# Kernel optimization log

Measured on AMD Instinct MI355X. Metric: run time of the kernel, lower is better.

The kernel has to match this reference:

```python
import jax, jax.numpy as jnp
import numpy as np

B, S, FDIM = 8, 512, 512
SUB = 4
DIM = FDIM // SUB            # 128 (reformer model dim)
HEADS, LOCAL_HEADS = 8, 2
LSH_HEADS = HEADS - LOCAL_HEADS
DH = 64                      # dim_head
INNER = HEADS * DH           # 512
BUCKET = 64
N_HASHES = 4
MEM = 128                    # num_mem_kv
DEPTH = 2                    # cfg.selfatn.num_layers
T = S * SUB + MEM            # 2176 internal seq (tokens + mem kv)
NB = T // BUCKET             # 34 buckets (even)
WINDOW = BUCKET * 2          # local attention window = 128
SELF_VAL = -5e4              # TOKEN_SELF_ATTN_VALUE
NEG = -1e9


def _ln(x, g, b, eps=1e-5):
    m = jnp.mean(x, -1, keepdims=True)
    v = jnp.mean((x - m) ** 2, -1, keepdims=True)
    return (x - m) * jax.lax.rsqrt(v + eps) * g + b


def _pos_encoding(s, d):
    pos = jnp.arange(s, dtype=jnp.float32)[:, None]
    i = jnp.arange(d, dtype=jnp.float32)
    div = 10000.0 ** (2.0 * i / d)
    pe = jnp.zeros((s, d), jnp.float32)
    pe = pe.at[:, 0::2].set(jnp.sin(pos / div[0::2]))
    pe = pe.at[:, 1::2].set(jnp.cos(pos / div[1::2]))
    return pe


def _l2norm(x, eps=1e-12):
    n = jnp.linalg.norm(x, axis=-1, keepdims=True)
    return x / jnp.maximum(n, eps)


def _lsh_attn(qk, v, rot):
    # qk, v: [Bh, T, DH]; rot: [DH, N_HASHES, NB//2] random rotations
    Bh, t, d = qk.shape
    rv = jnp.einsum('btf,fhi->bhti', qk, rot)
    rv = jnp.concatenate([rv, -rv], axis=-1)               # [Bh, nh, t, NB]
    buckets = jnp.argmax(rv, axis=-1)
    buckets = buckets + (jnp.arange(N_HASHES) * NB)[None, :, None]
    buckets = buckets.reshape(Bh, N_HASHES * t)
    ticker = jnp.arange(N_HASHES * t) % t
    key = buckets * t + ticker                             # sort by (bucket, pos)
    perm = jnp.argsort(key, axis=-1)                       # stable
    undo = jnp.argsort(perm, axis=-1)
    st = perm % t                                          # source positions
    sqk = jnp.take_along_axis(qk, st[..., None], axis=1)
    sv = jnp.take_along_axis(v, st[..., None], axis=1)
    C = N_HASHES * NB
    bq_t = st.reshape(Bh, C, BUCKET)
    bq = sqk.reshape(Bh, C, BUCKET, d)
    bv = sv.reshape(Bh, C, BUCKET, d)
    bk = _l2norm(bq)                                       # shared-QK: normalized keys
    look = lambda x: jnp.concatenate([x, jnp.roll(x, 1, axis=1)], axis=2)
    bk, bv, bkv_t = look(bk), look(bv), look(bq_t)
    dots = jnp.einsum('bcie,bcje->bcij', bq, bk) * (d ** -0.5)
    dots = jnp.where(bq_t[..., None] < bkv_t[:, :, None, :], NEG, dots)      # causal
    dots = jnp.where(bq_t[..., None] == bkv_t[:, :, None, :], SELF_VAL, dots)  # self
    lse = jax.nn.logsumexp(dots, axis=-1, keepdims=True)
    bo = jnp.einsum('bcij,bcje->bcie', jnp.exp(dots - lse), bv)
    so = bo.reshape(Bh, N_HASHES * t, d)
    slog = lse.reshape(Bh, N_HASHES * t)
    o = jnp.take_along_axis(so, undo[..., None], axis=1).reshape(Bh, N_HASHES, t, d)
    logits = jnp.take_along_axis(slog, undo, axis=1).reshape(Bh, N_HASHES, t, 1)
    w = jnp.exp(logits - jax.nn.logsumexp(logits, axis=1, keepdims=True))
    return (o * w).sum(axis=1)


def _local_attn(q, v):
    # shared-QK causal local attention, look_backward=1; q, v: [Bh, T, DH]
    Bh, t, d = q.shape
    W = t // WINDOW
    k = _l2norm(q)
    bq = q.reshape(Bh, W, WINDOW, d)
    bk = k.reshape(Bh, W, WINDOW, d)
    bv = v.reshape(Bh, W, WINDOW, d)
    tt = jnp.arange(t).reshape(W, WINDOW)
    prev = lambda x: jnp.concatenate([jnp.zeros_like(x[:, :1]), x[:, :-1]], axis=1)
    bk2 = jnp.concatenate([prev(bk), bk], axis=2)          # [Bh, W, 2W, d]
    bv2 = jnp.concatenate([prev(bv), bv], axis=2)
    tprev = jnp.concatenate([jnp.full((1, WINDOW), -1), tt[:-1]], axis=0)
    bkv_t = jnp.concatenate([tprev, tt], axis=1)           # [W, 2*WINDOW]
    dots = jnp.einsum('bwie,bwje->bwij', bq, bk2) * (d ** -0.5)
    dots = jnp.where(tt[:, :, None] == bkv_t[:, None, :], SELF_VAL, dots)
    dots = jnp.where(tt[:, :, None] < bkv_t[:, None, :], NEG, dots)
    dots = jnp.where((bkv_t == -1)[:, None, :], NEG, dots)
    attn = jax.nn.softmax(dots, axis=-1)
    return jnp.einsum('bwij,bwje->bwie', attn, bv2).reshape(Bh, t, d)


def _attn_layer(x, w_qk, w_v, mem_kv, w_out, b_out, rot):
    b, t0, _ = x.shape
    mem = jnp.broadcast_to(mem_kv, (b, MEM, DIM))
    xm = jnp.concatenate([x, mem], axis=1)                 # [b, T, DIM]
    qk = (xm @ w_qk).reshape(b, T, HEADS, DH).transpose(0, 2, 1, 3)
    v = (xm @ w_v).reshape(b, T, HEADS, DH).transpose(0, 2, 1, 3)
    merge = lambda a: a.reshape(-1, T, DH)
    out_loc = _local_attn(merge(qk[:, :LOCAL_HEADS]), merge(v[:, :LOCAL_HEADS]))
    out_lsh = _lsh_attn(merge(qk[:, LOCAL_HEADS:]), merge(v[:, LOCAL_HEADS:]), rot)
    out = jnp.concatenate([out_loc.reshape(b, LOCAL_HEADS, T, DH),
                           out_lsh.reshape(b, LSH_HEADS, T, DH)], axis=1)
    out = out.transpose(0, 2, 1, 3).reshape(b, T, INNER)
    return out[:, :t0] @ w_out + b_out


def setup_inputs() -> dict:
    key = jax.random.key(0)
    ks = jax.random.split(key, 20)
    std = 0.01  # init_network truncated-normal std
    p = lambda k, sh: std * jax.random.truncated_normal(k, -2.0, 2.0, sh, jnp.float32)
    return {
        'features': jax.random.normal(ks[0], (B, S, FDIM), jnp.float32),
        'w_qk': p(ks[1], (DEPTH, DIM, INNER)),
        'w_v': p(ks[2], (DEPTH, DIM, INNER)),
        'mem_kv': p(ks[3], (DEPTH, MEM, DIM)),
        'w_out': p(ks[4], (DEPTH, INNER, DIM)),
        'b_out': p(ks[5], (DEPTH, DIM)),
        'ln1_g': jnp.ones((DEPTH, DIM), jnp.float32),
        'ln1_b': jnp.zeros((DEPTH, DIM), jnp.float32),
        'ff_w1': p(ks[6], (DEPTH, DIM, 4 * DIM)),
        'ff_b1': p(ks[7], (DEPTH, 4 * DIM)),
        'ff_w2': p(ks[8], (DEPTH, 4 * DIM, DIM)),
        'ff_b2': p(ks[9], (DEPTH, DIM)),
        'ln2_g': jnp.ones((DEPTH, DIM), jnp.float32),
        'ln2_b': jnp.zeros((DEPTH, DIM), jnp.float32),
        'lnf_g': jnp.ones((DIM,), jnp.float32),
        'lnf_b': jnp.zeros((DIM,), jnp.float32),
        'rotations': jax.random.normal(ks[10], (DEPTH, DH, N_HASHES, NB // 2), jnp.float32),
    }


def reference(features, w_qk, w_v, mem_kv, w_out, b_out, ln1_g, ln1_b,
              ff_w1, ff_b1, ff_w2, ff_b2, ln2_g, ln2_b, lnf_g, lnf_b, rotations):
    b, s, fd = features.shape
    x = features + _pos_encoding(s, fd)                    # PositionalEncoding
    x = x.reshape(b, s * SUB, fd // SUB)                   # subspace split
    # reversible Reformer blocks: y1 = x1 + attn(ln(x2)); y2 = x2 + ff(ln(y1))
    x1, x2 = x, x
    for i in range(DEPTH):
        a_in = _ln(x2, ln1_g[i], ln1_b[i])
        y1 = x1 + _attn_layer(a_in, w_qk[i], w_v[i], mem_kv[i], w_out[i], b_out[i], rotations[i])
        g_in = _ln(y1, ln2_g[i], ln2_b[i])
        h = jax.nn.gelu(g_in @ ff_w1[i] + ff_b1[i], approximate=False)
        y2 = x2 + (h @ ff_w2[i] + ff_b2[i])
        x1, x2 = y1, y2
    x = 0.5 * (x1 + x2)                                    # mean of the two streams
    x = _ln(x, lnf_g, lnf_b)                               # final norm
    x = x.reshape(b, s, fd)                                # merge subspaces back
    return x.mean(axis=1)                                  # AvgPool
```

## Files before the change

### kernel.cpp

```cpp
#include <hip/hip_runtime.h>
#include <math.h>

#define NB_ 34
#define NEGV  (-1e9f)
#define SELFV (-5e4f)

typedef __attribute__((ext_vector_type(8))) short short8;
typedef __attribute__((ext_vector_type(4))) float floatx4;

__device__ __forceinline__ unsigned short f2bf(float f) {
  unsigned int u = __float_as_uint(f);
  u += 0x7fffu + ((u >> 16) & 1u);
  return (unsigned short)(u >> 16);
}
__device__ __forceinline__ float bflo(unsigned int u) { return __uint_as_float(u << 16); }
__device__ __forceinline__ float bfhi(unsigned int u) { return __uint_as_float(u & 0xffff0000u); }

__device__ __forceinline__ void load_row64(const float* __restrict__ p, float* q) {
#pragma unroll
  for (int d4 = 0; d4 < 16; ++d4) {
    float4 f = ((const float4*)p)[d4];
    q[d4*4+0]=f.x; q[d4*4+1]=f.y; q[d4*4+2]=f.z; q[d4*4+3]=f.w;
  }
}


__global__ void pos_kernel(const float* __restrict__ feat, float* __restrict__ x1,
                           float* __restrict__ x2) {
  int idx = blockIdx.x*256 + threadIdx.x;
  int d = idx & 127, t = (idx >> 7) & 2047, b = idx >> 18;
  int s = t >> 2, c = ((t & 3) << 7) | d;
  float div = powf(10000.0f, (float)c * (1.0f/256.0f));
  float arg = (float)s / div;
  float pe = (c & 1) ? cosf(arg) : sinf(arg);
  float val = feat[((size_t)b*512 + s)*512 + c] + pe;
  x1[idx] = val; x2[idx] = val;
}

__global__ __launch_bounds__(256) void ln_kernel(
    const float* __restrict__ in, const float* __restrict__ in2,
    const float* __restrict__ g, const float* __restrict__ bta,
    void* __restrict__ out, int rows, int ou, int oa, int obf) {
  int wid = threadIdx.x >> 6, lane = threadIdx.x & 63;
  int row = blockIdx.x*4 + wid;
  if (row >= rows) return;
  float2 x = ((const float2*)(in + (size_t)row*128))[lane];
  if (in2) {
    float2 y = ((const float2*)(in2 + (size_t)row*128))[lane];
    x.x = 0.5f*(x.x + y.x); x.y = 0.5f*(x.y + y.y);
  }
  float s = x.x + x.y;
#pragma unroll
  for (int m = 1; m < 64; m <<= 1) s += __shfl_xor(s, m, 64);
  float mean = s * (1.0f/128.0f);
  float dx = x.x - mean, dy = x.y - mean;
  float v = dx*dx + dy*dy;
#pragma unroll
  for (int m = 1; m < 64; m <<= 1) v += __shfl_xor(v, m, 64);
  float inv = 1.0f / sqrtf(v*(1.0f/128.0f) + 1e-5f);
  int orow = (ou == oa) ? row : (row/ou)*oa + (row%ou);
  float2 gg = ((const float2*)g)[lane];
  float2 bb = ((const float2*)bta)[lane];
  float ox = dx*inv*gg.x + bb.x, oy = dy*inv*gg.y + bb.y;
  if (obf) {
    ((unsigned int*)out)[(size_t)orow*64 + lane] =
        (unsigned int)f2bf(ox) | ((unsigned int)f2bf(oy) << 16);
  } else {
    float2 o; o.x = ox; o.y = oy;
    ((float2*)((float*)out + (size_t)orow*128))[lane] = o;
  }
}

__global__ void memfill_kernel(const float* __restrict__ mem,
                               unsigned short* __restrict__ xmb) {
  int idx = blockIdx.x*256 + threadIdx.x;
  int d = idx & 127, r = (idx >> 7) & 127, b = idx >> 14;
  xmb[((size_t)b*2176 + 2048 + r)*128 + d] = f2bf(mem[(r << 7) | d]);
}

__global__ void wconv_kernel(const float* __restrict__ w, unsigned short* __restrict__ wt,
                             int K, int N) {
  int idx = blockIdx.x*256 + threadIdx.x;
  int k = idx % K, n = idx / K;
  wt[idx] = f2bf(w[(size_t)k*N + n]);
}

__global__ __launch_bounds__(256) void gemm_bf16(
    const unsigned short* __restrict__ A, const unsigned short* __restrict__ Wt,
    const float* __restrict__ bias, const float* __restrict__ resid,
    float* __restrict__ C, unsigned short* __restrict__ Cb,
    int M, int N, int K, int au, int aa, int act) {
  __shared__ __align__(16) unsigned short As[64*40];
  __shared__ __align__(16) unsigned short Bs[64*40];
  int tid = threadIdx.x;
  int wid = tid >> 6, l15 = tid & 15, quad = (tid & 63) >> 4;
  int mb = blockIdx.y, nb = blockIdx.x;
  int r = tid >> 2, cc = (tid & 3)*8;
  int rg = mb*64 + r;
  int rp = (au == aa) ? rg : (rg/au)*aa + (rg%au);
  const unsigned short* arow = A + (size_t)rp*K + cc;
  const unsigned short* brow = Wt + (size_t)(nb*64 + r)*K + cc;
  floatx4 acc[4];
#pragma unroll
  for (int mt = 0; mt < 4; ++mt) acc[mt] = (floatx4){0.f,0.f,0.f,0.f};
  for (int k0 = 0; k0 < K; k0 += 32) {
    *(short8*)&As[r*40 + cc] = *(const short8*)(arow + k0);
    *(short8*)&Bs[r*40 + cc] = *(const short8*)(brow + k0);
    __syncthreads();
    short8 bfr = *(const short8*)&Bs[(wid*16 + l15)*40 + quad*8];
#pragma unroll
    for (int mt = 0; mt < 4; ++mt) {
      short8 afr = *(const short8*)&As[(mt*16 + l15)*40 + quad*8];
      acc[mt] = __builtin_amdgcn_mfma_f32_16x16x32_bf16(afr, bfr, acc[mt], 0, 0, 0);
    }
    __syncthreads();
  }
  int n = nb*64 + wid*16 + l15;
  float bi = bias ? bias[n] : 0.f;
#pragma unroll
  for (int mt = 0; mt < 4; ++mt) {
#pragma unroll
    for (int rr = 0; rr < 4; ++rr) {
      int m = mb*64 + mt*16 + quad*4 + rr;
      float val = acc[mt][rr] + bi;
      if (act) val = 0.5f*val*(1.0f + erff(val*0.70710678118654752f));
      if (resid) val += resid[(size_t)m*N + n];
      if (Cb) Cb[(size_t)m*N + n] = f2bf(val);
      else    C[(size_t)m*N + n] = val;
    }
  }
}

__global__ __launch_bounds__(128) void local_attn_mfma(
    const float* __restrict__ qk, const unsigned short* __restrict__ vbb,
    unsigned short* __restrict__ opart, float* __restrict__ lpart) {
  __shared__ __align__(16) unsigned short qq[128*72];
  __shared__ __align__(16) unsigned short kk[128*72];
  __shared__ __align__(16) unsigned short vt[64*136];
  __shared__ __align__(16) unsigned short ptile[2][16*136];
  __shared__ float invn[128];

  int blk = blockIdx.x;
  int part = blk & 1;
  int bw = blk >> 1;
  int bh = bw / 17, w = bw % 17;
  int b = bh >> 1, coloff = (bh & 1)*64;
  int tid = threadIdx.x;
  int t_qbase = w*128;

  unsigned short* obase = opart + (size_t)(part*16 + bh)*2176*64;
  float* lbase = lpart + (size_t)(part*16 + bh)*2176;

  if (part == 0 && w == 0) {
    uint4 z = {0,0,0,0};
    uint4* orow = (uint4*)(obase + (size_t)tid*64);
#pragma unroll
    for (int j = 0; j < 8; ++j) orow[j] = z;
    lbase[tid] = -1e9f;
    return;
  }

  {
    int t = t_qbase + tid;
    const float* qr = qk + ((size_t)(b*2176 + t)*512 + coloff);
    float ss = 0.f;
#pragma unroll
    for (int k8 = 0; k8 < 8; ++k8) {
      float4 a = ((const float4*)qr)[2*k8];
      float4 c = ((const float4*)qr)[2*k8+1];
      ss += a.x*a.x + a.y*a.y + a.z*a.z + a.w*a.w
          + c.x*c.x + c.y*c.y + c.z*c.z + c.w*c.w;
      short8 s8;
      s8[0]=(short)f2bf(a.x); s8[1]=(short)f2bf(a.y);
      s8[2]=(short)f2bf(a.z); s8[3]=(short)f2bf(a.w);
      s8[4]=(short)f2bf(c.x); s8[5]=(short)f2bf(c.y);
      s8[6]=(short)f2bf(c.z); s8[7]=(short)f2bf(c.w);
      *(short8*)&qq[tid*72 + k8*8] = s8;
    }
    if (part) invn[tid] = 1.0f / fmaxf(sqrtf(ss), 1e-12f);
  }
  if (part == 0) {
    int t = t_qbase - 128 + tid;
    const float* qr = qk + ((size_t)(b*2176 + t)*512 + coloff);
    float ss = 0.f;
#pragma unroll
    for (int k8 = 0; k8 < 8; ++k8) {
      float4 a = ((const float4*)qr)[2*k8];
      float4 c = ((const float4*)qr)[2*k8+1];
      ss += a.x*a.x + a.y*a.y + a.z*a.z + a.w*a.w
          + c.x*c.x + c.y*c.y + c.z*c.z + c.w*c.w;
      short8 s8;
      s8[0]=(short)f2bf(a.x); s8[1]=(short)f2bf(a.y);
      s8[2]=(short)f2bf(a.z); s8[3]=(short)f2bf(a.w);
      s8[4]=(short)f2bf(c.x); s8[5]=(short)f2bf(c.y);
      s8[6]=(short)f2bf(c.z); s8[7]=(short)f2bf(c.w);
      *(short8*)&kk[tid*72 + k8*8] = s8;
    }
    invn[tid] = 1.0f / fmaxf(sqrtf(ss), 1e-12f);
  }
  if (tid < 64) {
    int tkb = part ? t_qbase : (t_qbase - 128);
    const unsigned short* vrA = vbb + ((size_t)(b*2176 + tkb + 2*tid)*512 + coloff);
    const unsigned short* vrB = vrA + 512;
    unsigned int* vt32 = (unsigned int*)vt;
#pragma unroll
    for (int k = 0; k < 8; ++k) {
      uint4 ua = ((const uint4*)vrA)[k];
      uint4 uc = ((const uint4*)vrB)[k];
      const unsigned short* pa = (const unsigned short*)&ua;
      const unsigned short* pc = (const unsigned short*)&uc;
#pragma unroll
      for (int j = 0; j < 8; ++j) {
        int d = 8*k + j;
        vt32[d*68 + tid] = (unsigned int)pa[j] | ((unsigned int)pc[j] << 16);
      }
    }
  }
  __syncthreads();

  int wid = tid >> 6, l15 = tid & 15, quad = (tid & 63) >> 4;
  const unsigned short* keyrows = part ? qq : kk;
  int tkbase = part ? t_qbase : (t_qbase - 128);
  float sm8[8];
#pragma unroll
  for (int nt = 0; nt < 8; ++nt) sm8[nt] = invn[nt*16 + l15] * 0.125f;
  int qrow0 = wid*64;
  unsigned short* pt = &ptile[wid][0];

#pragma unroll
  for (int mt = 0; mt < 4; ++mt) {
    floatx4 acc[8];
#pragma unroll
    for (int nt = 0; nt < 8; ++nt) acc[nt] = (floatx4){0.f,0.f,0.f,0.f};
#pragma unroll
    for (int ks = 0; ks < 2; ++ks) {
      short8 afr = *(const short8*)&qq[(qrow0 + mt*16 + l15)*72 + ks*32 + quad*8];
#pragma unroll
      for (int nt = 0; nt < 8; ++nt) {
        short8 bfr = *(const short8*)&keyrows[(nt*16 + l15)*72 + ks*32 + quad*8];
        acc[nt] = __builtin_amdgcn_mfma_f32_16x16x32_bf16(afr, bfr, acc[nt], 0, 0, 0);
      }
    }
    float invl[4];
#pragma unroll
    for (int r = 0; r < 4; ++r) {
      int row = qrow0 + mt*16 + quad*4 + r;
      int t_q = t_qbase + row;
      float sv[8]; float mx = -INFINITY;
#pragma unroll
      for (int nt = 0; nt < 8; ++nt) {
        float sc = acc[nt][r] * sm8[nt];
        int t_k = tkbase + nt*16 + l15;
        sc = (t_k > t_q) ? NEGV : (t_k == t_q ? SELFV : sc);
        sv[nt] = sc; mx = fmaxf(mx, sc);
      }
#pragma unroll
      for (int m2 = 1; m2 < 16; m2 <<= 1) mx = fmaxf(mx, __shfl_xor(mx, m2, 64));
      float l = 0.f;
#pragma unroll
      for (int nt = 0; nt < 8; ++nt) { float pe = expf(sv[nt] - mx); sv[nt] = pe; l += pe; }
#pragma unroll
      for (int m2 = 1; m2 < 16; m2 <<= 1) l += __shfl_xor(l, m2, 64);
      invl[r] = 1.0f / l;
#pragma unroll
      for (int nt = 0; nt < 8; ++nt)
        pt[(quad*4 + r)*136 + nt*16 + l15] = f2bf(sv[nt]);
      if (l15 == 0) lbase[t_q] = mx + logf(l);
    }
#pragma unroll
    for (int nt = 0; nt < 4; ++nt) {
      floatx4 po = (floatx4){0.f,0.f,0.f,0.f};
#pragma unroll
      for (int ks = 0; ks < 4; ++ks) {
        short8 afr = *(const short8*)&pt[l15*136 + ks*32 + quad*8];
        short8 bfr = *(const short8*)&vt[(nt*16 + l15)*136 + ks*32 + quad*8];
        po = __builtin_amdgcn_mfma_f32_16x16x32_bf16(afr, bfr, po, 0, 0, 0);
      }
      int d = nt*16 + l15;
#pragma unroll
      for (int r = 0; r < 4; ++r) {
        int t_q = t_qbase + qrow0 + mt*16 + quad*4 + r;
        obase[(size_t)t_q*64 + d] = f2bf(po[r] * invl[r]);
      }
    }
  }
}

__global__ void local_comb(const unsigned short* __restrict__ opart,
                           const float* __restrict__ lpart,
                           unsigned short* __restrict__ aob) {
  int idx = blockIdx.x*256 + threadIdx.x;
  if (idx >= 16*2176*8) return;
  int f8 = idx & 7;
  int p  = (idx >> 3) % 2176;
  int bh = idx / (8*2176);
  float lg0 = lpart[(size_t)bh*2176 + p];
  float lg1 = lpart[(size_t)(16 + bh)*2176 + p];
  float m = fmaxf(lg0, lg1);
  float e0 = expf(lg0 - m), e1 = expf(lg1 - m);
  float inv = 1.0f / (e0 + e1);
  float w0 = e0*inv, w1 = e1*inv;
  uint4 u0 = ((const uint4*)(opart + ((size_t)bh*2176 + p)*64))[f8];
  uint4 u1 = ((const uint4*)(opart + ((size_t)(16 + bh)*2176 + p)*64))[f8];
  uint4 o;
  o.x = (unsigned int)f2bf(w0*bflo(u0.x) + w1*bflo(u1.x)) |
        ((unsigned int)f2bf(w0*bfhi(u0.x) + w1*bfhi(u1.x)) << 16);
  o.y = (unsigned int)f2bf(w0*bflo(u0.y) + w1*bflo(u1.y)) |
        ((unsigned int)f2bf(w0*bfhi(u0.y) + w1*bfhi(u1.y)) << 16);
  o.z = (unsigned int)f2bf(w0*bflo(u0.z) + w1*bflo(u1.z)) |
        ((unsigned int)f2bf(w0*bfhi(u0.z) + w1*bfhi(u1.z)) << 16);
  o.w = (unsigned int)f2bf(w0*bflo(u0.w) + w1*bflo(u1.w)) |
        ((unsigned int)f2bf(w0*bfhi(u0.w) + w1*bfhi(u1.w)) << 16);
  int b = bh >> 1;
  ((uint4*)(aob + ((size_t)(b*2176 + p)*512 + (bh & 1)*64 + f8*8)))[0] = o;
}

__global__ __launch_bounds__(256) void hash_kernel(
    const float* __restrict__ qk, const float* __restrict__ rot, int* __restrict__ bucket) {
  __shared__ float rl[64*68];
  for (int l = threadIdx.x; l < 4352; l += 256) rl[l] = rot[l];
  __syncthreads();
  int idx = blockIdx.x*256 + threadIdx.x;
  int p = idx % 2176, bh = idx / 2176;
  int b = bh / 6, hh = bh % 6;
  float q[64];
  load_row64(qk + ((size_t)(b*2176 + p)*512 + (2+hh)*64), q);
  for (int h = 0; h < 4; ++h) {
    float rv[17];
#pragma unroll
    for (int k = 0; k < 17; ++k) rv[k] = 0.f;
    for (int d = 0; d < 64; ++d) {
      float qd = q[d];
      const float* rp = &rl[d*68 + h*17];
#pragma unroll
      for (int k = 0; k < 17; ++k) rv[k] = fmaf(qd, rp[k], rv[k]);
    }
    float best = rv[0]; int bi = 0;
#pragma unroll
    for (int k = 1; k < 34; ++k) {
      float val = (k < 17) ? rv[k] : -rv[k-17];
      if (val > best) { best = val; bi = k; }
    }
    bucket[(size_t)(bh*4 + h)*2176 + p] = bi;
  }
}

__global__ __launch_bounds__(256) void sort_kernel(const int* __restrict__ bucket,
                                                   int* __restrict__ st) {
  __shared__ int sb[2176];
  __shared__ int cnt[NB_*256];
  __shared__ int csum[256];
  int tid = threadIdx.x;
  int bhh = blockIdx.x;
  const int* bin = bucket + (size_t)bhh*2176;
  for (int p = tid; p < 2176; p += 256) sb[p] = bin[p];
#pragma unroll
  for (int j = 0; j < NB_; ++j) cnt[j*256 + tid] = 0;
  __syncthreads();
  int s0 = tid*9;
  int e = s0 + 9; if (e > 2176) e = 2176;
  for (int p = s0; p < e; ++p) cnt[sb[p]*256 + tid] += 1;
  __syncthreads();
  {
    int sum = 0;
    int base0 = tid*NB_;
#pragma unroll
    for (int j = 0; j < NB_; ++j) {
      int v = cnt[base0 + j];
      cnt[base0 + j] = sum;
      sum += v;
    }
    csum[tid] = sum;
  }
  __syncthreads();
  for (int off = 1; off < 256; off <<= 1) {
    int v = (tid >= off) ? csum[tid - off] : 0;
    __syncthreads();
    csum[tid] += v;
    __syncthreads();
  }
  {
    int base = tid ? csum[tid-1] : 0;
    int base0 = tid*NB_;
#pragma unroll
    for (int j = 0; j < NB_; ++j) cnt[base0 + j] += base;
  }
  __syncthreads();
  int bh = bhh >> 2, h = bhh & 3;
  int* outp = st + (size_t)bh*8704 + h*2176;
  for (int p = s0; p < e; ++p) {
    int bk = sb[p];
    int r = cnt[bk*256 + tid]++;
    outp[r] = p;
  }
}

__global__ __launch_bounds__(128) void lsh_attn_mfma(
    const float* __restrict__ qk, const unsigned short* __restrict__ vbb,
    const int* __restrict__ st, unsigned short* __restrict__ o_all,
    float* __restrict__ logits) {
  __shared__ __align__(16) unsigned short qq[192*72];
  __shared__ __align__(16) unsigned short vt[64*200];
  __shared__ __align__(16) unsigned short ptile[2][16*136];
  __shared__ int   tkl[192];
  __shared__ float invn[192];

  int blk = blockIdx.x;
  int bh = blk / 68, pair = blk % 68;
  int c0 = pair*2;
  int b = bh / 6, coloff = (2 + bh % 6)*64;
  int tid = threadIdx.x;

#pragma unroll
  for (int rr = 0; rr < 2; ++rr) {
    if (rr == 1 && tid >= 64) break;
    int r = (rr == 0) ? tid : 128 + tid;
    int cr = c0 - 1 + (r >> 6); if (cr < 0) cr += 136;
    int p = st[(size_t)bh*8704 + cr*64 + (r & 63)];
    tkl[r] = p;
    const float* qr = qk + ((size_t)(b*2176 + p)*512 + coloff);
    float ss = 0.f;
#pragma unroll
    for (int k8 = 0; k8 < 8; ++k8) {
      float4 a = ((const float4*)qr)[2*k8];
      float4 c = ((const float4*)qr)[2*k8+1];
      ss += a.x*a.x + a.y*a.y + a.z*a.z + a.w*a.w
          + c.x*c.x + c.y*c.y + c.z*c.z + c.w*c.w;
      short8 s8;
      s8[0]=(short)f2bf(a.x); s8[1]=(short)f2bf(a.y);
      s8[2]=(short)f2bf(a.z); s8[3]=(short)f2bf(a.w);
      s8[4]=(short)f2bf(c.x); s8[5]=(short)f2bf(c.y);
      s8[6]=(short)f2bf(c.z); s8[7]=(short)f2bf(c.w);
      *(short8*)&qq[r*72 + k8*8] = s8;
    }
    invn[r] = 1.0f / fmaxf(sqrtf(ss), 1e-12f);
  }
  if (tid < 96) {
    int r0 = 2*tid, r1 = r0 + 1;
    int cr0 = c0 - 1 + (r0 >> 6); if (cr0 < 0) cr0 += 136;
    int cr1 = c0 - 1 + (r1 >> 6); if (cr1 < 0) cr1 += 136;
    int p0 = st[(size_t)bh*8704 + cr0*64 + (r0 & 63)];
    int p1 = st[(size_t)bh*8704 + cr1*64 + (r1 & 63)];
    const unsigned short* a = vbb + ((size_t)(b*2176 + p0)*512 + coloff);
    const unsigned short* c = vbb + ((size_t)(b*2176 + p1)*512 + coloff);
    unsigned int* vt32 = (unsigned int*)vt;
#pragma unroll
    for (int k = 0; k < 8; ++k) {
      uint4 ua = ((const uint4*)a)[k];
      uint4 uc = ((const uint4*)c)[k];
      const unsigned short* pa = (const unsigned short*)&ua;
      const unsigned short* pc = (const unsigned short*)&uc;
#pragma unroll
      for (int j = 0; j < 8; ++j) {
        int d = 8*k + j;
        vt32[d*100 + tid] = (unsigned int)pa[j] | ((unsigned int)pc[j] << 16);
      }
    }
  }
  __syncthreads();

  int wid = tid >> 6, l15 = tid & 15, quad = (tid & 63) >> 4;
  int kbase = wid*64, qbase = 64 + wid*64;
  int c = c0 + wid;
  int h = c / NB_;
  float sm8[8]; int tk8[8];
#pragma unroll
  for (int nt = 0; nt < 8; ++nt) {
    int kr = kbase + nt*16 + l15;
    sm8[nt] = invn[kr] * 0.125f;
    tk8[nt] = tkl[kr];
  }
  float* logrow = logits + (size_t)(bh*4 + h)*2176;
  unsigned short* obase = o_all + (size_t)(bh*4 + h)*2176*64;
  unsigned short* pt = &ptile[wid][0];

#pragma unroll
  for (int mt = 0; mt < 4; ++mt) {
    floatx4 acc[8];
#pragma unroll
    for (int nt = 0; nt < 8; ++nt) acc[nt] = (floatx4){0.f,0.f,0.f,0.f};
#pragma unroll
    for (int ks = 0; ks < 2; ++ks) {
      short8 afr = *(const short8*)&qq[(qbase + mt*16 + l15)*72 + ks*32 + quad*8];
#pragma unroll
      for (int nt = 0; nt < 8; ++nt) {
        short8 bfr = *(const short8*)&qq[(kbase + nt*16 + l15)*72 + ks*32 + quad*8];
        acc[nt] = __builtin_amdgcn_mfma_f32_16x16x32_bf16(afr, bfr, acc[nt], 0, 0, 0);
      }
    }
    float invl[4];
#pragma unroll
    for (int r = 0; r < 4; ++r) {
      int t_q = tkl[qbase + mt*16 + quad*4 + r];
      float sv8[8]; float mx = -INFINITY;
#pragma unroll
      for (int nt = 0; nt < 8; ++nt) {
        float sc = acc[nt][r] * sm8[nt];
        int t_k = tk8[nt];
        sc = (t_k > t_q) ? NEGV : (t_k == t_q ? SELFV : sc);
        sv8[nt] = sc; mx = fmaxf(mx, sc);
      }
#pragma unroll
      for (int m2 = 1; m2 < 16; m2 <<= 1) mx = fmaxf(mx, __shfl_xor(mx, m2, 64));
      float l = 0.f;
#pragma unroll
      for (int nt = 0; nt < 8; ++nt) { float pe = expf(sv8[nt] - mx); sv8[nt] = pe; l += pe; }
#pragma unroll
      for (int m2 = 1; m2 < 16; m2 <<= 1) l += __shfl_xor(l, m2, 64);
      invl[r] = 1.0f / l;
#pragma unroll
      for (int nt = 0; nt < 8; ++nt)
        pt[(quad*4 + r)*136 + nt*16 + l15] = f2bf(sv8[nt]);
      if (l15 == 0) logrow[t_q] = mx + logf(l);
    }
#pragma unroll
    for (int nt = 0; nt < 4; ++nt) {
      floatx4 po = (floatx4){0.f,0.f,0.f,0.f};
#pragma unroll
      for (int ks = 0; ks < 4; ++ks) {
        short8 afr = *(const short8*)&pt[l15*136 + ks*32 + quad*8];
        short8 bfr = *(const short8*)&vt[(nt*16 + l15)*200 + kbase + ks*32 + quad*8];
        po = __builtin_amdgcn_mfma_f32_16x16x32_bf16(afr, bfr, po, 0, 0, 0);
      }
      int d = nt*16 + l15;
#pragma unroll
      for (int r = 0; r < 4; ++r) {
        int p_q = tkl[qbase + mt*16 + quad*4 + r];
        obase[(size_t)p_q*64 + d] = f2bf(po[r] * invl[r]);
      }
    }
  }
}

__global__ void comb_kernel(const unsigned short* __restrict__ o_all,
                            const float* __restrict__ logits,
                            unsigned short* __restrict__ aob) {
  int idx = blockIdx.x*256 + threadIdx.x;
  int f8 = idx & 7;
  int p  = (idx >> 3) % 2176;
  int bh = idx / (8*2176);
  float lg0 = logits[(size_t)(bh*4+0)*2176 + p];
  float lg1 = logits[(size_t)(bh*4+1)*2176 + p];
  float lg2 = logits[(size_t)(bh*4+2)*2176 + p];
  float lg3 = logits[(size_t)(bh*4+3)*2176 + p];
  float m = fmaxf(fmaxf(lg0, lg1), fmaxf(lg2, lg3));
  float e0 = expf(lg0-m), e1 = expf(lg1-m), e2 = expf(lg2-m), e3 = expf(lg3-m);
  float inv = 1.0f / (e0+e1+e2+e3);
  float wh[4] = {e0*inv, e1*inv, e2*inv, e3*inv};
  float o[8];
#pragma unroll
  for (int d = 0; d < 8; ++d) o[d] = 0.f;
#pragma unroll
  for (int h = 0; h < 4; ++h) {
    float wg = wh[h];
    uint4 u = ((const uint4*)(o_all + ((size_t)(bh*4+h)*2176 + p)*64))[f8];
    o[0] = fmaf(wg, bflo(u.x), o[0]); o[1] = fmaf(wg, bfhi(u.x), o[1]);
    o[2] = fmaf(wg, bflo(u.y), o[2]); o[3] = fmaf(wg, bfhi(u.y), o[3]);
    o[4] = fmaf(wg, bflo(u.z), o[4]); o[5] = fmaf(wg, bfhi(u.z), o[5]);
    o[6] = fmaf(wg, bflo(u.w), o[6]); o[7] = fmaf(wg, bfhi(u.w), o[7]);
  }
  int b = bh / 6, hh = bh % 6;
  uint4 u;
  u.x = (unsigned int)f2bf(o[0]) | ((unsigned int)f2bf(o[1]) << 16);
  u.y = (unsigned int)f2bf(o[2]) | ((unsigned int)f2bf(o[3]) << 16);
  u.z = (unsigned int)f2bf(o[4]) | ((unsigned int)f2bf(o[5]) << 16);
  u.w = (unsigned int)f2bf(o[6]) | ((unsigned int)f2bf(o[7]) << 16);
  ((uint4*)(aob + ((size_t)(b*2176 + p)*512 + (2+hh)*64 + f8*8)))[0] = u;
}

__global__ void pool_kernel(const float* __restrict__ xln, float* __restrict__ out) {
  int idx = blockIdx.x*256 + threadIdx.x;
  int c = idx & 511, b = idx >> 9;
  int sub = c >> 7, d = c & 127;
  const float* p = xln + ((size_t)b*2048 + sub)*128 + d;
  float s = 0.f;
  for (int i = 0; i < 512; ++i) s += p[(size_t)i*512];
  out[idx] = s * (1.0f/512.0f);
}

#define OFF_X1    0ull
#define OFF_X2    2097152ull
#define OFF_XM    4194304ull
#define OFF_XMB   6422528ull
#define OFF_QKB   7536640ull
#define OFF_VB    16449536ull
#define OFF_AOB   25362432ull
#define OFF_OALL  29818880ull
#define OFF_LOG   43188224ull
#define OFF_BKT   43606016ull
#define OFF_ST    44023808ull
#define OFF_WTB   44441600ull
#define WS_FLOATS 44769280ull

extern "C" void kernel_launch(void* const* d_in, const int* in_sizes, int n_in,
                              void* d_out, int out_size, void* d_ws, size_t ws_size,
                              hipStream_t stream) {
  (void)in_sizes; (void)n_in; (void)out_size;
  if (ws_size < WS_FLOATS * 4ull) return;

  const float* feat  = (const float*)d_in[0];
  const float* w_qk  = (const float*)d_in[1];
  const float* w_v   = (const float*)d_in[2];
  const float* memkv = (const float*)d_in[3];
  const float* w_out = (const float*)d_in[4];
  const float* b_out = (const float*)d_in[5];
  const float* ln1g  = (const float*)d_in[6];
  const float* ln1b  = (const float*)d_in[7];
  const float* ffw1  = (const float*)d_in[8];
  const float* ffb1  = (const float*)d_in[9];
  const float* ffw2  = (const float*)d_in[10];
  const float* ffb2  = (const float*)d_in[11];
  const float* ln2g  = (const float*)d_in[12];
  const float* ln2b  = (const float*)d_in[13];
  const float* lnfg  = (const float*)d_in[14];
  const float* lnfb  = (const float*)d_in[15];
  const float* rots  = (const float*)d_in[16];

  float* ws = (float*)d_ws;
  float* x1   = ws + OFF_X1;
  float* x2   = ws + OFF_X2;
  float* xm   = ws + OFF_XM;
  unsigned short* xmb = (unsigned short*)(ws + OFF_XMB);
  float* qkb  = ws + OFF_QKB;
  unsigned short* vbb = (unsigned short*)(ws + OFF_VB);
  unsigned short* aob = (unsigned short*)(ws + OFF_AOB);
  unsigned short* hb  = (unsigned short*)(ws + OFF_AOB);
  unsigned short* oall = (unsigned short*)(ws + OFF_OALL);
  unsigned short* opart = (unsigned short*)(ws + OFF_OALL);
  float* lpart = ws + OFF_OALL + 2228224ull;
  float* logi = ws + OFF_LOG;
  int*   bkt  = (int*)(ws + OFF_BKT);
  int*   st   = (int*)(ws + OFF_ST);
  unsigned short* wtb = (unsigned short*)(ws + OFF_WTB);
  float* outp = (float*)d_out;

  pos_kernel<<<8192, 256, 0, stream>>>(feat, x1, x2);

  for (int i = 0; i < 2; ++i) {
    wconv_kernel<<<256, 256, 0, stream>>>(w_qk + i*65536, wtb + (i*5+0)*65536, 128, 512);
    wconv_kernel<<<256, 256, 0, stream>>>(w_v  + i*65536, wtb + (i*5+1)*65536, 128, 512);
    wconv_kernel<<<256, 256, 0, stream>>>(w_out+ i*65536, wtb + (i*5+2)*65536, 512, 128);
    wconv_kernel<<<256, 256, 0, stream>>>(ffw1 + i*65536, wtb + (i*5+3)*65536, 128, 512);
    wconv_kernel<<<256, 256, 0, stream>>>(ffw2 + i*65536, wtb + (i*5+4)*65536, 512, 128);
  }

  for (int i = 0; i < 2; ++i) {
    const unsigned short* Wqk = wtb + (i*5+0)*65536;
    const unsigned short* Wv  = wtb + (i*5+1)*65536;
    const unsigned short* Wo  = wtb + (i*5+2)*65536;
    const unsigned short* W1  = wtb + (i*5+3)*65536;
    const unsigned short* W2  = wtb + (i*5+4)*65536;

    ln_kernel<<<4096, 256, 0, stream>>>(x2, nullptr, ln1g + i*128, ln1b + i*128,
                                        xmb, 16384, 2048, 2176, 1);
    memfill_kernel<<<512, 256, 0, stream>>>(memkv + i*16384, xmb);

    gemm_bf16<<<dim3(8, 272), 256, 0, stream>>>(xmb, Wqk, nullptr, nullptr, qkb, nullptr,
                                                17408, 512, 128, 1, 1, 0);
    gemm_bf16<<<dim3(8, 272), 256, 0, stream>>>(xmb, Wv, nullptr, nullptr, nullptr, vbb,
                                                17408, 512, 128, 1, 1, 0);

    local_attn_mfma<<<544, 128, 0, stream>>>(qkb, vbb, opart, lpart);
    local_comb<<<1088, 256, 0, stream>>>(opart, lpart, aob);

    hash_kernel<<<408, 256, 0, stream>>>(qkb, rots + i*4352, bkt);
    sort_kernel<<<192, 256, 0, stream>>>(bkt, st);
    lsh_attn_mfma<<<3264, 128, 0, stream>>>(qkb, vbb, st, oall, logi);
    comb_kernel<<<3264, 256, 0, stream>>>(oall, logi, aob);

    gemm_bf16<<<dim3(2, 256), 256, 0, stream>>>(aob, Wo, b_out + i*128, x1, x1, nullptr,
                                                16384, 128, 512, 2048, 2176, 0);
    ln_kernel<<<4096, 256, 0, stream>>>(x1, nullptr, ln2g + i*128, ln2b + i*128,
                                        xmb, 16384, 1, 1, 1);
    gemm_bf16<<<dim3(8, 256), 256, 0, stream>>>(xmb, W1, ffb1 + i*512, nullptr, nullptr, hb,
                                                16384, 512, 128, 1, 1, 1);
    gemm_bf16<<<dim3(2, 256), 256, 0, stream>>>(hb, W2, ffb2 + i*128, x2, x2, nullptr,
                                                16384, 128, 512, 1, 1, 0);
  }

  ln_kernel<<<4096, 256, 0, stream>>>(x1, x2, lnfg, lnfb, xm, 16384, 1, 1, 0);
  pool_kernel<<<16, 256, 0, stream>>>(xm, outp);
}
```

Baseline: 872.0 us.

## Store QK in bf16, fuse QK/V GEMMs, precompute key norms, parallelize pooling

The QK and V projections are merged into one GEMM kernel that writes both outputs in bf16. It relies on the two converted weight blocks sitting next to each other in memory. A separate kernel computes the inverse L2 norm of each QK row once, so the local and LSH attention kernels and the hash kernel no longer reload fp32 rows, recompute norms and convert to bf16. The pooling kernel now uses one wavefront per output with a shuffle reduction instead of a long serial loop per thread. Hashing and norms now read bf16-rounded QK, which can move a few bucket assignments.

```diff
diff --git a/kernel.cpp b/kernel.cpp
--- a/kernel.cpp
+++ b/kernel.cpp
@@ -16,11 +16,14 @@
 __device__ __forceinline__ float bflo(unsigned int u) { return __uint_as_float(u << 16); }
 __device__ __forceinline__ float bfhi(unsigned int u) { return __uint_as_float(u & 0xffff0000u); }
 
-__device__ __forceinline__ void load_row64(const float* __restrict__ p, float* q) {
-#pragma unroll
-  for (int d4 = 0; d4 < 16; ++d4) {
-    float4 f = ((const float4*)p)[d4];
-    q[d4*4+0]=f.x; q[d4*4+1]=f.y; q[d4*4+2]=f.z; q[d4*4+3]=f.w;
+__device__ __forceinline__ void load_row64_bf(const unsigned short* __restrict__ p, float* q) {
+#pragma unroll
+  for (int k = 0; k < 8; ++k) {
+    uint4 u = ((const uint4*)p)[k];
+    q[8*k+0]=bflo(u.x); q[8*k+1]=bfhi(u.x);
+    q[8*k+2]=bflo(u.y); q[8*k+3]=bfhi(u.y);
+    q[8*k+4]=bflo(u.z); q[8*k+5]=bfhi(u.z);
+    q[8*k+6]=bflo(u.w); q[8*k+7]=bfhi(u.w);
   }
 }
 
@@ -131,8 +134,67 @@
   }
 }
 
+__global__ __launch_bounds__(256) void gemm_qv(
+    const unsigned short* __restrict__ A, const unsigned short* __restrict__ Wt,
+    unsigned short* __restrict__ Q, unsigned short* __restrict__ V) {
+  __shared__ __align__(16) unsigned short As[64*40];
+  __shared__ __align__(16) unsigned short Bs[64*40];
+  int tid = threadIdx.x;
+  int wid = tid >> 6, l15 = tid & 15, quad = (tid & 63) >> 4;
+  int mb = blockIdx.y, nb = blockIdx.x;
+  int r = tid >> 2, cc = (tid & 3)*8;
+  const unsigned short* arow = A + (size_t)(mb*64 + r)*128 + cc;
+  const unsigned short* brow = Wt + (size_t)(nb*64 + r)*128 + cc;
+  floatx4 acc[4];
+#pragma unroll
+  for (int mt = 0; mt < 4; ++mt) acc[mt] = (floatx4){0.f,0.f,0.f,0.f};
+#pragma unroll
+  for (int k0 = 0; k0 < 128; k0 += 32) {
+    *(short8*)&As[r*40 + cc] = *(const short8*)(arow + k0);
+    *(short8*)&Bs[r*40 + cc] = *(const short8*)(brow + k0);
+    __syncthreads();
+    short8 bfr = *(const short8*)&Bs[(wid*16 + l15)*40 + quad*8];
+#pragma unroll
+    for (int mt = 0; mt < 4; ++mt) {
+      short8 afr = *(const short8*)&As[(mt*16 + l15)*40 + quad*8];
+      acc[mt] = __builtin_amdgcn_mfma_f32_16x16x32_bf16(afr, bfr, acc[mt], 0, 0, 0);
+    }
+    __syncthreads();
+  }
+  int n = nb*64 + wid*16 + l15;
+#pragma unroll
+  for (int mt = 0; mt < 4; ++mt) {
+#pragma unroll
+    for (int rr = 0; rr < 4; ++rr) {
+      int m = mb*64 + mt*16 + quad*4 + rr;
+      unsigned short bv = f2bf(acc[mt][rr]);
+      if (n < 512) Q[(size_t)m*512 + n] = bv;
+      else         V[(size_t)m*512 + (n - 512)] = bv;
+    }
+  }
+}
+
+__global__ __launch_bounds__(256) void norm_kernel(const unsigned short* __restrict__ qkb,
+                                                   float* __restrict__ nrm) {
+  int idx = blockIdx.x*256 + threadIdx.x;
+  int head = idx & 7, row = idx >> 3;
+  const uint4* src = (const uint4*)(qkb + (size_t)row*512 + head*64);
+  float ss = 0.f;
+#pragma unroll
+  for (int k = 0; k < 8; ++k) {
+    uint4 u = src[k];
+    ss += bflo(u.x)*bflo(u.x) + bfhi(u.x)*bfhi(u.x)
+        + bflo(u.y)*bflo(u.y) + bfhi(u.y)*bfhi(u.y)
+        + bflo(u.z)*bflo(u.z) + bfhi(u.z)*bfhi(u.z)
+        + bflo(u.w)*bflo(u.w) + bfhi(u.w)*bfhi(u.w);
+  }
+  int b = row / 2176, t = row % 2176;
+  nrm[((size_t)b*8 + head)*2176 + t] = 1.0f / fmaxf(sqrtf(ss), 1e-12f);
+}
+
 __global__ __launch_bounds__(128) void local_attn_mfma(
-    const float* __restrict__ qk, const unsigned short* __restrict__ vbb,
+    const unsigned short* __restrict__ qkb, const unsigned short* __restrict__ vbb,
+    const float* __restrict__ nrm,
     unsigned short* __restrict__ opart, float* __restrict__ lpart) {
   __shared__ __align__(16) unsigned short qq[128*72];
   __shared__ __align__(16) unsigned short kk[128*72];
@@ -160,47 +222,22 @@
     return;
   }
 
+  int tkbase = part ? t_qbase : (t_qbase - 128);
+  const float* nrmh = nrm + ((size_t)b*8 + (bh & 1))*2176;
+  invn[tid] = nrmh[tkbase + tid];
+
   {
-    int t = t_qbase + tid;
-    const float* qr = qk + ((size_t)(b*2176 + t)*512 + coloff);
-    float ss = 0.f;
-#pragma unroll
-    for (int k8 = 0; k8 < 8; ++k8) {
-      float4 a = ((const float4*)qr)[2*k8];
-      float4 c = ((const float4*)qr)[2*k8+1];
-      ss += a.x*a.x + a.y*a.y + a.z*a.z + a.w*a.w
-          + c.x*c.x + c.y*c.y + c.z*c.z + c.w*c.w;
-      short8 s8;
-      s8[0]=(short)f2bf(a.x); s8[1]=(short)f2bf(a.y);
-      s8[2]=(short)f2bf(a.z); s8[3]=(short)f2bf(a.w);
-      s8[4]=(short)f2bf(c.x); s8[5]=(short)f2bf(c.y);
-      s8[6]=(short)f2bf(c.z); s8[7]=(short)f2bf(c.w);
-      *(short8*)&qq[tid*72 + k8*8] = s8;
-    }
-    if (part) invn[tid] = 1.0f / fmaxf(sqrtf(ss), 1e-12f);
+    const unsigned short* qr = qkb + ((size_t)(b*2176 + t_qbase + tid)*512 + coloff);
+#pragma unroll
+    for (int k = 0; k < 8; ++k) *(uint4*)&qq[tid*72 + k*8] = ((const uint4*)qr)[k];
   }
   if (part == 0) {
-    int t = t_qbase - 128 + tid;
-    const float* qr = qk + ((size_t)(b*2176 + t)*512 + coloff);
-    float ss = 0.f;
-#pragma unroll
-    for (int k8 = 0; k8 < 8; ++k8) {
-      float4 a = ((const float4*)qr)[2*k8];
-      float4 c = ((const float4*)qr)[2*k8+1];
-      ss += a.x*a.x + a.y*a.y + a.z*a.z + a.w*a.w
-          + c.x*c.x + c.y*c.y + c.z*c.z + c.w*c.w;
-      short8 s8;
-      s8[0]=(short)f2bf(a.x); s8[1]=(short)f2bf(a.y);
-      s8[2]=(short)f2bf(a.z); s8[3]=(short)f2bf(a.w);
-      s8[4]=(short)f2bf(c.x); s8[5]=(short)f2bf(c.y);
-      s8[6]=(short)f2bf(c.z); s8[7]=(short)f2bf(c.w);
-      *(short8*)&kk[tid*72 + k8*8] = s8;
-    }
-    invn[tid] = 1.0f / fmaxf(sqrtf(ss), 1e-12f);
+    const unsigned short* qr = qkb + ((size_t)(b*2176 + t_qbase - 128 + tid)*512 + coloff);
+#pragma unroll
+    for (int k = 0; k < 8; ++k) *(uint4*)&kk[tid*72 + k*8] = ((const uint4*)qr)[k];
   }
   if (tid < 64) {
-    int tkb = part ? t_qbase : (t_qbase - 128);
-    const unsigned short* vrA = vbb + ((size_t)(b*2176 + tkb + 2*tid)*512 + coloff);
+    const unsigned short* vrA = vbb + ((size_t)(b*2176 + tkbase + 2*tid)*512 + coloff);
     const unsigned short* vrB = vrA + 512;
     unsigned int* vt32 = (unsigned int*)vt;
 #pragma unroll
@@ -220,7 +257,6 @@
 
   int wid = tid >> 6, l15 = tid & 15, quad = (tid & 63) >> 4;
   const unsigned short* keyrows = part ? qq : kk;
-  int tkbase = part ? t_qbase : (t_qbase - 128);
   float sm8[8];
 #pragma unroll
   for (int nt = 0; nt < 8; ++nt) sm8[nt] = invn[nt*16 + l15] * 0.125f;
@@ -316,7 +352,8 @@
 }
 
 __global__ __launch_bounds__(256) void hash_kernel(
-    const float* __restrict__ qk, const float* __restrict__ rot, int* __restrict__ bucket) {
+    const unsigned short* __restrict__ qkb, const float* __restrict__ rot,
+    int* __restrict__ bucket) {
   __shared__ float rl[64*68];
   for (int l = threadIdx.x; l < 4352; l += 256) rl[l] = rot[l];
   __syncthreads();
@@ -324,7 +361,7 @@
   int p = idx % 2176, bh = idx / 2176;
   int b = bh / 6, hh = bh % 6;
   float q[64];
-  load_row64(qk + ((size_t)(b*2176 + p)*512 + (2+hh)*64), q);
+  load_row64_bf(qkb + ((size_t)(b*2176 + p)*512 + (2+hh)*64), q);
   for (int h = 0; h < 4; ++h) {
     float rv[17];
 #pragma unroll
@@ -396,9 +433,9 @@
 }
 
 __global__ __launch_bounds__(128) void lsh_attn_mfma(
-    const float* __restrict__ qk, const unsigned short* __restrict__ vbb,
-    const int* __restrict__ st, unsigned short* __restrict__ o_all,
-    float* __restrict__ logits) {
+    const unsigned short* __restrict__ qkb, const unsigned short* __restrict__ vbb,
+    const float* __restrict__ nrm, const int* __restrict__ st,
+    unsigned short* __restrict__ o_all, float* __restrict__ logits) {
   __shared__ __align__(16) unsigned short qq[192*72];
   __shared__ __align__(16) unsigned short vt[64*200];
   __shared__ __align__(16) unsigned short ptile[2][16*136];
@@ -410,6 +447,7 @@
   int c0 = pair*2;
   int b = bh / 6, coloff = (2 + bh % 6)*64;
   int tid = threadIdx.x;
+  const float* nrmh = nrm + ((size_t)b*8 + 2 + bh % 6)*2176;
 
 #pragma unroll
   for (int rr = 0; rr < 2; ++rr) {
@@ -418,22 +456,10 @@
     int cr = c0 - 1 + (r >> 6); if (cr < 0) cr += 136;
     int p = st[(size_t)bh*8704 + cr*64 + (r & 63)];
     tkl[r] = p;
-    const float* qr = qk + ((size_t)(b*2176 + p)*512 + coloff);
-    float ss = 0.f;
-#pragma unroll
-    for (int k8 = 0; k8 < 8; ++k8) {
-      float4 a = ((const float4*)qr)[2*k8];
-      float4 c = ((const float4*)qr)[2*k8+1];
-      ss += a.x*a.x + a.y*a.y + a.z*a.z + a.w*a.w
-          + c.x*c.x + c.y*c.y + c.z*c.z + c.w*c.w;
-      short8 s8;
-      s8[0]=(short)f2bf(a.x); s8[1]=(short)f2bf(a.y);
-      s8[2]=(short)f2bf(a.z); s8[3]=(short)f2bf(a.w);
-      s8[4]=(short)f2bf(c.x); s8[5]=(short)f2bf(c.y);
-      s8[6]=(short)f2bf(c.z); s8[7]=(short)f2bf(c.w);
-      *(short8*)&qq[r*72 + k8*8] = s8;
-    }
-    invn[r] = 1.0f / fmaxf(sqrtf(ss), 1e-12f);
+    invn[r] = nrmh[p];
+    const unsigned short* qr = qkb + ((size_t)(b*2176 + p)*512 + coloff);
+#pragma unroll
+    for (int k = 0; k < 8; ++k) *(uint4*)&qq[r*72 + k*8] = ((const uint4*)qr)[k];
   }
   if (tid < 96) {
     int r0 = 2*tid, r1 = r0 + 1;
@@ -568,14 +594,19 @@
   ((uint4*)(aob + ((size_t)(b*2176 + p)*512 + (2+hh)*64 + f8*8)))[0] = u;
 }
 
-__global__ void pool_kernel(const float* __restrict__ xln, float* __restrict__ out) {
-  int idx = blockIdx.x*256 + threadIdx.x;
-  int c = idx & 511, b = idx >> 9;
+__global__ __launch_bounds__(256) void pool_kernel(const float* __restrict__ xln,
+                                                   float* __restrict__ out) {
+  int o = blockIdx.x*4 + (threadIdx.x >> 6);
+  int lane = threadIdx.x & 63;
+  int c = o & 511, b = o >> 9;
   int sub = c >> 7, d = c & 127;
   const float* p = xln + ((size_t)b*2048 + sub)*128 + d;
   float s = 0.f;
-  for (int i = 0; i < 512; ++i) s += p[(size_t)i*512];
-  out[idx] = s * (1.0f/512.0f);
+#pragma unroll
+  for (int j = 0; j < 8; ++j) s += p[(size_t)(lane + 64*j)*512];
+#pragma unroll
+  for (int m = 1; m < 64; m <<= 1) s += __shfl_xor(s, m, 64);
+  if (lane == 0) out[o] = s * (1.0f/512.0f);
 }
 
 #define OFF_X1    0ull
@@ -590,7 +621,8 @@
 #define OFF_BKT   43606016ull
 #define OFF_ST    44023808ull
 #define OFF_WTB   44441600ull
-#define WS_FLOATS 44769280ull
+#define OFF_NRM   44769280ull
+#define WS_FLOATS 44908544ull
 
 extern "C" void kernel_launch(void* const* d_in, const int* in_sizes, int n_in,
                               void* d_out, int out_size, void* d_ws, size_t ws_size,
@@ -621,7 +653,7 @@
   float* x2   = ws + OFF_X2;
   float* xm   = ws + OFF_XM;
   unsigned short* xmb = (unsigned short*)(ws + OFF_XMB);
-  float* qkb  = ws + OFF_QKB;
+  unsigned short* qkb = (unsigned short*)(ws + OFF_QKB);
   unsigned short* vbb = (unsigned short*)(ws + OFF_VB);
   unsigned short* aob = (unsigned short*)(ws + OFF_AOB);
   unsigned short* hb  = (unsigned short*)(ws + OFF_AOB);
@@ -632,6 +664,7 @@
   int*   bkt  = (int*)(ws + OFF_BKT);
   int*   st   = (int*)(ws + OFF_ST);
   unsigned short* wtb = (unsigned short*)(ws + OFF_WTB);
+  float* nrm  = ws + OFF_NRM;
   float* outp = (float*)d_out;
 
   pos_kernel<<<8192, 256, 0, stream>>>(feat, x1, x2);
@@ -645,8 +678,7 @@
   }
 
   for (int i = 0; i < 2; ++i) {
-    const unsigned short* Wqk = wtb + (i*5+0)*65536;
-    const unsigned short* Wv  = wtb + (i*5+1)*65536;
+    const unsigned short* Wqv = wtb + (i*5+0)*65536;
     const unsigned short* Wo  = wtb + (i*5+2)*65536;
     const unsigned short* W1  = wtb + (i*5+3)*65536;
     const unsigned short* W2  = wtb + (i*5+4)*65536;
@@ -655,17 +687,15 @@
                                         xmb, 16384, 2048, 2176, 1);
     memfill_kernel<<<512, 256, 0, stream>>>(memkv + i*16384, xmb);
 
-    gemm_bf16<<<dim3(8, 272), 256, 0, stream>>>(xmb, Wqk, nullptr, nullptr, qkb, nullptr,
-                                                17408, 512, 128, 1, 1, 0);
-    gemm_bf16<<<dim3(8, 272), 256, 0, stream>>>(xmb, Wv, nullptr, nullptr, nullptr, vbb,
-                                                17408, 512, 128, 1, 1, 0);
-
-    local_attn_mfma<<<544, 128, 0, stream>>>(qkb, vbb, opart, lpart);
+    gemm_qv<<<dim3(16, 272), 256, 0, stream>>>(xmb, Wqv, qkb, vbb);
+    norm_kernel<<<544, 256, 0, stream>>>(qkb, nrm);
+
+    local_attn_mfma<<<544, 128, 0, stream>>>(qkb, vbb, nrm, opart, lpart);
     local_comb<<<1088, 256, 0, stream>>>(opart, lpart, aob);
 
     hash_kernel<<<408, 256, 0, stream>>>(qkb, rots + i*4352, bkt);
     sort_kernel<<<192, 256, 0, stream>>>(bkt, st);
-    lsh_attn_mfma<<<3264, 128, 0, stream>>>(qkb, vbb, st, oall, logi);
+    lsh_attn_mfma<<<3264, 128, 0, stream>>>(qkb, vbb, nrm, st, oall, logi);
     comb_kernel<<<3264, 256, 0, stream>>>(oall, logi, aob);
 
     gemm_bf16<<<dim3(2, 256), 256, 0, stream>>>(aob, Wo, b_out + i*128, x1, x1, nullptr,
@@ -679,5 +709,5 @@
   }
 
   ln_kernel<<<4096, 256, 0, stream>>>(x1, x2, lnfg, lnfb, xm, 16384, 1, 1, 0);
-  pool_kernel<<<16, 256, 0, stream>>>(xm, outp);
-}
+  pool_kernel<<<1024, 256, 0, stream>>>(xm, outp);
+}
```

Measured after the change: 763.3 us. 1.14x faster.
